# Kernel optimization log

Measured on AMD Instinct MI355X. Metric: run time of the kernel, lower is better.

## Reference

```python
import jax, jax.numpy as jnp
import numpy as np

N_EMBD = 2048
N_HEAD = 16
N_HIDDEN = 5632  # find_multiple(int(2*4*2048/3), 256)
EPS = 1e-5
BETA = 1.0


def rmsnorm(x, scale):
    # mean of squares computed in fp32 as in the torch code
    norm = jnp.mean(x.astype(jnp.float32) ** 2, axis=-1, keepdims=True)
    x_normed = x * jax.lax.rsqrt(norm + EPS)
    return (scale * x_normed).astype(x.dtype)


def setup_inputs() -> dict:
    key = jax.random.key(0)
    ks = jax.random.split(key, 9)
    B, T, C = 1, 2048, N_EMBD
    s = lambda k, shape, fan: jax.random.normal(k, shape, jnp.float32) * (1.0 / np.sqrt(fan))
    return {
        "x": jax.random.normal(ks[0], (B, T, C), jnp.float32),
        "alibi": jax.random.normal(ks[1], (N_HEAD, T, T), jnp.float32),
        "w_attn": s(ks[2], (C, 3 * C), C),   # c_attn weight (in, out) layout
        "w_proj": s(ks[3], (C, C), C),
        "w_fc1": s(ks[4], (C, N_HIDDEN), C),
        "w_fc2": s(ks[5], (C, N_HIDDEN), C),
        "w_mlp_proj": s(ks[6], (N_HIDDEN, C), N_HIDDEN),
        "rms1_scale": jnp.ones((C,), jnp.float32),
        "rms2_scale": jnp.ones((C,), jnp.float32),
    }


def attention(x, alibi, w_attn, w_proj):
    B, T, C = x.shape
    hd = C // N_HEAD
    qkv = x @ w_attn  # [B,T,3C]
    q, k, v = jnp.split(qkv, 3, axis=-1)
    q = q.reshape(B, T, N_HEAD, hd).transpose(0, 2, 1, 3)  # [B,H,T,hd]
    k = k.reshape(B, T, N_HEAD, hd).transpose(0, 2, 1, 3)
    v = v.reshape(B, T, N_HEAD, hd).transpose(0, 2, 1, 3)
    scale = 1.0 / np.sqrt(hd)
    scores = jnp.einsum("bhqd,bhkd->bhqk", q, k) * scale + BETA * alibi  # [B,H,T,T]
    causal = jnp.tril(jnp.ones((T, T), bool))
    scores = jnp.where(causal, scores, -jnp.inf)
    attn = jax.nn.softmax(scores, axis=-1)
    y = jnp.einsum("bhqk,bhkd->bhqd", attn, v)
    y = y.transpose(0, 2, 1, 3).reshape(B, T, C)
    return y @ w_proj


def mlp(x, w_fc1, w_fc2, w_mlp_proj):
    return (jax.nn.silu(x @ w_fc1) * (x @ w_fc2)) @ w_mlp_proj


def reference(x, alibi, w_attn, w_proj, w_fc1, w_fc2, w_mlp_proj, rms1_scale, rms2_scale):
    x = x + attention(rmsnorm(x, rms1_scale), alibi, w_attn, w_proj)
    x = x + mlp(rmsnorm(x, rms2_scale), w_fc1, w_fc2, w_mlp_proj)
    return x
```

## Files before the change

### kernel.cpp

```cpp
#include <hip/hip_runtime.h>
#include <stdint.h>

typedef __attribute__((ext_vector_type(4))) float f32x4;
typedef __attribute__((ext_vector_type(8))) __bf16 bf8_t;
typedef __attribute__((ext_vector_type(8))) uint16_t u16x8;

typedef __attribute__((address_space(1))) uint8_t as1_u8;
typedef __attribute__((address_space(3))) uint8_t as3_u8;

__device__ inline void async_copy16(const void* g, void* l) {
  __builtin_amdgcn_global_load_lds((const as1_u8*)g, (as3_u8*)l, 16, 0, 0);
}

__device__ inline uint16_t f2bf(float f) {
  uint32_t u = __builtin_bit_cast(uint32_t, f);
  u = (u + 0x7fff + ((u >> 16) & 1)) >> 16;
  return (uint16_t)u;
}
__device__ inline float bf2f(uint16_t h) {
  uint32_t u = ((uint32_t)h) << 16;
  return __builtin_bit_cast(float, u);
}
__device__ inline int swz(int r) { return (((r & 7) ^ ((r >> 3) & 7)) << 4); }
__device__ inline int vswz(int r) { return ((r & 7) << 4); }

__global__ __launch_bounds__(256) void rmsnorm_kernel(const float* __restrict__ X,
                                                      const float* __restrict__ S,
                                                      uint16_t* __restrict__ O) {
  const int row = blockIdx.x;
  const int tid = threadIdx.x;
  const float* xr = X + (size_t)row * 2048;
  float4 v1 = ((const float4*)xr)[tid * 2];
  float4 v2 = ((const float4*)xr)[tid * 2 + 1];
  float ss = v1.x * v1.x + v1.y * v1.y + v1.z * v1.z + v1.w * v1.w +
             v2.x * v2.x + v2.y * v2.y + v2.z * v2.z + v2.w * v2.w;
  #pragma unroll
  for (int m = 1; m < 64; m <<= 1) ss += __shfl_xor(ss, m);
  __shared__ float wsum[4];
  if ((tid & 63) == 0) wsum[tid >> 6] = ss;
  __syncthreads();
  float tot = wsum[0] + wsum[1] + wsum[2] + wsum[3];
  float inv = rsqrtf(tot * (1.0f / 2048.0f) + 1e-5f);
  const int base = tid * 8;
  const float* sc = S + base;
  float xs[8] = {v1.x, v1.y, v1.z, v1.w, v2.x, v2.y, v2.z, v2.w};
  u16x8 o;
  #pragma unroll
  for (int j = 0; j < 8; j++) o[j] = f2bf(xs[j] * inv * sc[j]);
  *(u16x8*)(O + (size_t)row * 2048 + base) = o;
}

__device__ inline void transpose_tile2(const float* __restrict__ W, uint16_t* __restrict__ WT,
                                       int K, int N, int bx, int by, int tid, int catoff) {
  __shared__ float tile[64][65];
  const int n0 = bx * 64, k0 = by * 64;
  const int lr = tid >> 4;
  const int lc = (tid & 15) * 4;
  #pragma unroll
  for (int i = 0; i < 4; i++) {
    const float4 v = *(const float4*)&W[(size_t)(k0 + lr + i * 16) * N + n0 + lc];
    tile[lr + i * 16][lc] = v.x;
    tile[lr + i * 16][lc + 1] = v.y;
    tile[lr + i * 16][lc + 2] = v.z;
    tile[lr + i * 16][lc + 3] = v.w;
  }
  __syncthreads();
  const int tn = tid >> 3;
  const int tk = (tid & 7) * 8;
  #pragma unroll
  for (int i = 0; i < 2; i++) {
    u16x8 o;
    #pragma unroll
    for (int j = 0; j < 8; j++) o[j] = f2bf(tile[tk + j][tn + i * 32]);
    const int n = n0 + tn + i * 32;
    const int row = (catoff < 0) ? n : (((n >> 4) << 5) + catoff + (n & 15));
    *(u16x8*)&WT[(size_t)row * K + k0 + tk] = o;
  }
}

__global__ __launch_bounds__(256) void transpose_all(
    const float* __restrict__ w_attn, const float* __restrict__ w_proj,
    const float* __restrict__ w_fc1, const float* __restrict__ w_fc2,
    const float* __restrict__ w_mp,
    uint16_t* __restrict__ wt_attn, uint16_t* __restrict__ wt_proj,
    uint16_t* __restrict__ wt_cat, uint16_t* __restrict__ wt_mp) {
  int idx = blockIdx.x;
  const int tid = threadIdx.x;
  if (idx < 3072) {
    transpose_tile2(w_attn, wt_attn, 2048, 6144, idx % 96, idx / 96, tid, -1);
  } else if (idx < 4096) {
    idx -= 3072;
    transpose_tile2(w_proj, wt_proj, 2048, 2048, idx % 32, idx / 32, tid, -1);
  } else if (idx < 6912) {
    idx -= 4096;
    transpose_tile2(w_fc1, wt_cat, 2048, 5632, idx % 88, idx / 88, tid, 0);
  } else if (idx < 9728) {
    idx -= 6912;
    transpose_tile2(w_fc2, wt_cat, 2048, 5632, idx % 88, idx / 88, tid, 16);
  } else {
    idx -= 9728;
    transpose_tile2(w_mp, wt_mp, 5632, 2048, idx % 32, idx / 32, tid, -1);
  }
}

__global__ __launch_bounds__(256) void transpose_v(const uint16_t* __restrict__ qkv,
                                                   uint16_t* __restrict__ vT) {
  __shared__ uint16_t tile[64][68];
  const int t0 = blockIdx.x * 64;
  const int c0 = blockIdx.y * 64;
  const int tid = threadIdx.x;
  const int lr = tid >> 3;
  const int lc = (tid & 7) * 8;
  #pragma unroll
  for (int i = 0; i < 2; i++) {
    const int r = lr + i * 32;
    u16x8 v = *(const u16x8*)&qkv[(size_t)(t0 + r) * 6144 + 4096 + c0 + lc];
    #pragma unroll
    for (int j = 0; j < 8; j++) tile[lc + j][r] = v[j];
  }
  __syncthreads();
  #pragma unroll
  for (int i = 0; i < 2; i++) {
    const int c = lr + i * 32;
    u16x8 o = *(const u16x8*)&tile[c][lc];
    *(u16x8*)&vT[(size_t)(c0 + c) * 2048 + t0 + lc] = o;
  }
}

enum { EPI_BF16 = 0, EPI_ADDF32 = 1, EPI_SILUMUL = 2 };

__device__ inline void gemm_epi(int EPI, void* Cout, const void* RES, size_t idx, float v) {
  if (EPI == EPI_BF16) {
    ((uint16_t*)Cout)[idx] = f2bf(v);
  } else if (EPI == EPI_ADDF32) {
    ((float*)Cout)[idx] = ((const float*)RES)[idx] + v;
  } else {
    const float g = bf2f(((const uint16_t*)RES)[idx]);
    const float sg = g / (1.0f + __expf(-g));
    ((uint16_t*)Cout)[idx] = f2bf(sg * v);
  }
}

template <int EPI>
__global__ __launch_bounds__(256, 2) void gemm_bt(const uint16_t* __restrict__ A,
                                                  const uint16_t* __restrict__ BT,
                                                  void* __restrict__ Cout,
                                                  const void* __restrict__ RES,
                                                  int M, int N, int K) {
  __shared__ uint16_t As[128 * 64];
  __shared__ uint16_t Bs[128 * 64];
  const int tid = threadIdx.x;
  const int lane = tid & 63;
  const int w = tid >> 6;
  const int l15 = lane & 15, l4 = lane >> 4;
  const int m0 = blockIdx.y * 128, n0 = blockIdx.x * 128;
  const int wr = w >> 1, wc = w & 1;

  f32x4 acc[4][4];
  #pragma unroll
  for (int i = 0; i < 4; i++)
    #pragma unroll
    for (int j = 0; j < 4; j++) acc[i][j] = 0.0f;

  for (int kk = 0; kk < K; kk += 64) {
    __syncthreads();
    #pragma unroll
    for (int s = 0; s < 4; s++) {
      const int bu = s * 256 + w * 64;
      const int u = bu + lane;
      const int row = u >> 3;
      const int ch = (u & 7) ^ (row & 7);
      async_copy16(A + (size_t)(m0 + row) * K + kk + ch * 8, (char*)As + bu * 16);
      async_copy16(BT + (size_t)(n0 + row) * K + kk + ch * 8, (char*)Bs + bu * 16);
    }
    __syncthreads();
    bf8_t a[4][2], b[4][2];
    #pragma unroll
    for (int mi = 0; mi < 4; mi++)
      #pragma unroll
      for (int ks = 0; ks < 2; ks++) {
        const int R = wr * 64 + mi * 16 + l15;
        a[mi][ks] = *(const bf8_t*)((const char*)As + R * 128 + (((ks * 4 + l4) ^ (R & 7)) * 16));
      }
    #pragma unroll
    for (int ni = 0; ni < 4; ni++)
      #pragma unroll
      for (int ks = 0; ks < 2; ks++) {
        const int R = wc * 64 + ni * 16 + l15;
        b[ni][ks] = *(const bf8_t*)((const char*)Bs + R * 128 + (((ks * 4 + l4) ^ (R & 7)) * 16));
      }
    #pragma unroll
    for (int mi = 0; mi < 4; mi++)
      #pragma unroll
      for (int ni = 0; ni < 4; ni++)
        #pragma unroll
        for (int ks = 0; ks < 2; ks++)
          acc[mi][ni] = __builtin_amdgcn_mfma_f32_16x16x32_bf16(a[mi][ks], b[ni][ks],
                                                                acc[mi][ni], 0, 0, 0);
  }

  #pragma unroll
  for (int mi = 0; mi < 4; mi++) {
    #pragma unroll
    for (int ni = 0; ni < 4; ni++) {
      #pragma unroll
      for (int r = 0; r < 4; r++) {
        const int row = m0 + wr * 64 + mi * 16 + l4 * 4 + r;
        const int col = n0 + wc * 64 + ni * 16 + l15;
        gemm_epi(EPI, Cout, RES, (size_t)row * N + col, acc[mi][ni][r]);
      }
    }
  }
}

__global__ __launch_bounds__(256, 2) void gemm_cat(const uint16_t* __restrict__ A,
                                                   const uint16_t* __restrict__ BT,
                                                   uint16_t* __restrict__ Cout,
                                                   int M, int K) {
  __shared__ uint16_t As[128 * 64];
  __shared__ uint16_t Bs[128 * 64];
  const int tid = threadIdx.x;
  const int lane = tid & 63;
  const int w = tid >> 6;
  const int l15 = lane & 15, l4 = lane >> 4;
  const int m0 = blockIdx.y * 128, n0 = blockIdx.x * 128;
  const int wr = w >> 1, wc = w & 1;

  f32x4 acc[4][4];
  #pragma unroll
  for (int i = 0; i < 4; i++)
    #pragma unroll
    for (int j = 0; j < 4; j++) acc[i][j] = 0.0f;

  for (int kk = 0; kk < K; kk += 64) {
    __syncthreads();
    #pragma unroll
    for (int s = 0; s < 4; s++) {
      const int bu = s * 256 + w * 64;
      const int u = bu + lane;
      const int row = u >> 3;
      const int ch = (u & 7) ^ (row & 7);
      async_copy16(A + (size_t)(m0 + row) * K + kk + ch * 8, (char*)As + bu * 16);
      async_copy16(BT + (size_t)(n0 + row) * K + kk + ch * 8, (char*)Bs + bu * 16);
    }
    __syncthreads();
    bf8_t a[4][2], b[4][2];
    #pragma unroll
    for (int mi = 0; mi < 4; mi++)
      #pragma unroll
      for (int ks = 0; ks < 2; ks++) {
        const int R = wr * 64 + mi * 16 + l15;
        a[mi][ks] = *(const bf8_t*)((const char*)As + R * 128 + (((ks * 4 + l4) ^ (R & 7)) * 16));
      }
    #pragma unroll
    for (int ni = 0; ni < 4; ni++)
      #pragma unroll
      for (int ks = 0; ks < 2; ks++) {
        const int R = wc * 64 + ni * 16 + l15;
        b[ni][ks] = *(const bf8_t*)((const char*)Bs + R * 128 + (((ks * 4 + l4) ^ (R & 7)) * 16));
      }
    #pragma unroll
    for (int mi = 0; mi < 4; mi++)
      #pragma unroll
      for (int ni = 0; ni < 4; ni++)
        #pragma unroll
        for (int ks = 0; ks < 2; ks++)
          acc[mi][ni] = __builtin_amdgcn_mfma_f32_16x16x32_bf16(a[mi][ks], b[ni][ks],
                                                                acc[mi][ni], 0, 0, 0);
  }

  #pragma unroll
  for (int mi = 0; mi < 4; mi++) {
    #pragma unroll
    for (int p = 0; p < 2; p++) {
      const int col = n0 / 2 + ((wc * 4 + 2 * p) >> 1) * 16 + l15;
      #pragma unroll
      for (int r = 0; r < 4; r++) {
        const int row = m0 + wr * 64 + mi * 16 + l4 * 4 + r;
        const float g = acc[mi][2 * p][r];
        const float h = acc[mi][2 * p + 1][r];
        const float sg = g / (1.0f + __expf(-g));
        Cout[(size_t)row * 5632 + col] = f2bf(sg * h);
      }
    }
  }
}

template <int EPI>
__global__ __launch_bounds__(256, 3) void gemm_bt64(const uint16_t* __restrict__ A,
                                                    const uint16_t* __restrict__ BT,
                                                    void* __restrict__ Cout,
                                                    const void* __restrict__ RES,
                                                    int M, int N, int K) {
  __shared__ uint16_t As[128 * 64];
  __shared__ uint16_t Bs[64 * 64];
  const int tid = threadIdx.x;
  const int lane = tid & 63;
  const int w = tid >> 6;
  const int l15 = lane & 15, l4 = lane >> 4;
  const int m0 = blockIdx.y * 128, n0 = blockIdx.x * 64;

  f32x4 acc[2][4];
  #pragma unroll
  for (int i = 0; i < 2; i++)
    #pragma unroll
    for (int j = 0; j < 4; j++) acc[i][j] = 0.0f;

  for (int kk = 0; kk < K; kk += 64) {
    __syncthreads();
    #pragma unroll
    for (int s = 0; s < 4; s++) {
      const int bu = s * 256 + w * 64;
      const int u = bu + lane;
      const int row = u >> 3;
      const int ch = (u & 7) ^ (row & 7);
      async_copy16(A + (size_t)(m0 + row) * K + kk + ch * 8, (char*)As + bu * 16);
    }
    #pragma unroll
    for (int s = 0; s < 2; s++) {
      const int bu = s * 256 + w * 64;
      const int u = bu + lane;
      const int row = u >> 3;
      const int ch = (u & 7) ^ (row & 7);
      async_copy16(BT + (size_t)(n0 + row) * K + kk + ch * 8, (char*)Bs + bu * 16);
    }
    __syncthreads();
    bf8_t a[2][2], b[4][2];
    #pragma unroll
    for (int mi = 0; mi < 2; mi++)
      #pragma unroll
      for (int ks = 0; ks < 2; ks++) {
        const int R = w * 32 + mi * 16 + l15;
        a[mi][ks] = *(const bf8_t*)((const char*)As + R * 128 + (((ks * 4 + l4) ^ (R & 7)) * 16));
      }
    #pragma unroll
    for (int ni = 0; ni < 4; ni++)
      #pragma unroll
      for (int ks = 0; ks < 2; ks++) {
        const int R = ni * 16 + l15;
        b[ni][ks] = *(const bf8_t*)((const char*)Bs + R * 128 + (((ks * 4 + l4) ^ (R & 7)) * 16));
      }
    #pragma unroll
    for (int mi = 0; mi < 2; mi++)
      #pragma unroll
      for (int ni = 0; ni < 4; ni++)
        #pragma unroll
        for (int ks = 0; ks < 2; ks++)
          acc[mi][ni] = __builtin_amdgcn_mfma_f32_16x16x32_bf16(a[mi][ks], b[ni][ks],
                                                                acc[mi][ni], 0, 0, 0);
  }

  #pragma unroll
  for (int mi = 0; mi < 2; mi++) {
    #pragma unroll
    for (int ni = 0; ni < 4; ni++) {
      #pragma unroll
      for (int r = 0; r < 4; r++) {
        const int row = m0 + w * 32 + mi * 16 + l4 * 4 + r;
        const int col = n0 + ni * 16 + l15;
        gemm_epi(EPI, Cout, RES, (size_t)row * N + col, acc[mi][ni][r]);
      }
    }
  }
}

#define PART_STRIDE (64 * 128 + 128)
__global__ __launch_bounds__(256, 2) void attn_part(const uint16_t* __restrict__ qkv,
                                                    const uint16_t* __restrict__ vT,
                                                    const float* __restrict__ alibi,
                                                    float* __restrict__ part) {
  const int p = blockIdx.x;
  const int qt = 31 - blockIdx.y;
  const int h = blockIdx.z;
  const int c = (qt + 4) >> 2;
  const int start = p * c;
  const int end = min((p + 1) * c, qt + 1);
  if (start >= end) return;

  const int tid = threadIdx.x;
  const int lane = tid & 63;
  const int w = tid >> 6;
  const int l15 = lane & 15, l4 = lane >> 4;

  __shared__ uint16_t Ks[2][64 * 128];
  __shared__ uint16_t Vs[2][128 * 64];
  __shared__ uint16_t Ps[4][16 * 64];

  const float scale = 0.08838834764831845f;

  auto stage = [&](int kv0, int b) {
    #pragma unroll
    for (int i = 0; i < 4; i++) {
      const int u = tid + i * 256;
      const int r = u >> 4;
      const int cc = (u & 15) ^ ((r & 7) ^ ((r >> 3) & 7));
      async_copy16(qkv + (size_t)(kv0 + r) * 6144 + 2048 + h * 128 + cc * 8,
                   (char*)Ks[b] + u * 16);
    }
    #pragma unroll
    for (int i = 0; i < 4; i++) {
      const int u = tid + i * 256;
      const int r = u >> 3;
      const int cc = (u & 7) ^ (r & 7);
      async_copy16(vT + (size_t)(h * 128 + r) * 2048 + kv0 + cc * 8,
                   (char*)Vs[b] + u * 16);
    }
  };
  auto load_al = [&](int kv0, float (&al)[4][4]) {
    #pragma unroll
    for (int r = 0; r < 4; r++) {
      const size_t rowb = ((size_t)h * 2048 + (qt * 64 + w * 16 + l4 * 4 + r)) * 2048;
      #pragma unroll
      for (int nf = 0; nf < 4; nf++)
        al[nf][r] = alibi[rowb + kv0 + nf * 16 + l15];
    }
  };

  const int qrow = qt * 64 + w * 16 + l15;
  bf8_t qf[4];
  #pragma unroll
  for (int kc = 0; kc < 4; kc++)
    qf[kc] = *(const bf8_t*)(qkv + (size_t)qrow * 6144 + h * 128 + kc * 32 + l4 * 8);

  f32x4 accy[8];
  #pragma unroll
  for (int i = 0; i < 8; i++) accy[i] = 0.0f;
  float mrun[4], lrun[4];
  #pragma unroll
  for (int r = 0; r < 4; r++) { mrun[r] = -1e30f; lrun[r] = 0.0f; }

  stage(start * 64, 0);
  float al[4][4];
  load_al(start * 64, al);

  for (int kvt = start; kvt < end; kvt++) {
    const int b = (kvt - start) & 1;
    const int kv0 = kvt * 64;
    __syncthreads();

    const int kvn = (kvt + 1 < end) ? (kvt + 1) : kvt;
    float aln[4][4];
    load_al(kvn * 64, aln);
    stage(kvn * 64, b ^ 1);

    float s[4][4];
    #pragma unroll
    for (int nf = 0; nf < 4; nf++) {
      f32x4 sa = 0.0f;
      const int krow = nf * 16 + l15;
      __builtin_amdgcn_s_setprio(1);
      #pragma unroll
      for (int kc = 0; kc < 4; kc++) {
        bf8_t kb = *(const bf8_t*)((const char*)Ks[b] +
                                   ((krow * 256 + kc * 64 + l4 * 16) ^ swz(krow)));
        sa = __builtin_amdgcn_mfma_f32_16x16x32_bf16(qf[kc], kb, sa, 0, 0, 0);
      }
      __builtin_amdgcn_s_setprio(0);
      const int kvcol = kv0 + nf * 16 + l15;
      #pragma unroll
      for (int r = 0; r < 4; r++) {
        const int q = qt * 64 + w * 16 + l4 * 4 + r;
        float sv = sa[r] * scale + al[nf][r];
        if (kvcol > q) sv = -1e30f;
        s[nf][r] = sv;
      }
    }

    #pragma unroll
    for (int r = 0; r < 4; r++) {
      float rm = fmaxf(fmaxf(s[0][r], s[1][r]), fmaxf(s[2][r], s[3][r]));
      rm = fmaxf(rm, __shfl_xor(rm, 1));
      rm = fmaxf(rm, __shfl_xor(rm, 2));
      rm = fmaxf(rm, __shfl_xor(rm, 4));
      rm = fmaxf(rm, __shfl_xor(rm, 8));
      const float mnew = fmaxf(mrun[r], rm);
      const float alpha = __expf(mrun[r] - mnew);
      mrun[r] = mnew;
      float rs = 0.0f;
      #pragma unroll
      for (int nf = 0; nf < 4; nf++) {
        const float pp = __expf(s[nf][r] - mnew);
        s[nf][r] = pp;
        rs += pp;
      }
      rs += __shfl_xor(rs, 1);
      rs += __shfl_xor(rs, 2);
      rs += __shfl_xor(rs, 4);
      rs += __shfl_xor(rs, 8);
      lrun[r] = lrun[r] * alpha + rs;
      #pragma unroll
      for (int df = 0; df < 8; df++) accy[df][r] *= alpha;
    }

    #pragma unroll
    for (int nf = 0; nf < 4; nf++) {
      #pragma unroll
      for (int r = 0; r < 4; r++) {
        const int rq = l4 * 4 + r;
        const int bo = (rq * 128 + (nf * 16 + l15) * 2) ^ vswz(rq);
        *(uint16_t*)((char*)Ps[w] + bo) = f2bf(s[nf][r]);
      }
    }

    __builtin_amdgcn_s_setprio(1);
    #pragma unroll
    for (int kk = 0; kk < 2; kk++) {
      bf8_t pa = *(const bf8_t*)((const char*)Ps[w] +
                                 ((l15 * 128 + kk * 64 + l4 * 16) ^ vswz(l15)));
      #pragma unroll
      for (int df = 0; df < 8; df++) {
        const int vr = df * 16 + l15;
        bf8_t vb = *(const bf8_t*)((const char*)Vs[b] +
                                   ((vr * 128 + kk * 64 + l4 * 16) ^ vswz(vr)));
        accy[df] = __builtin_amdgcn_mfma_f32_16x16x32_bf16(pa, vb, accy[df], 0, 0, 0);
      }
    }
    __builtin_amdgcn_s_setprio(0);

    #pragma unroll
    for (int nf = 0; nf < 4; nf++)
      #pragma unroll
      for (int r = 0; r < 4; r++) al[nf][r] = aln[nf][r];
  }

  float* pb = part + (size_t)(((h * 32 + qt) * 4) + p) * PART_STRIDE;
  #pragma unroll
  for (int df = 0; df < 8; df++) {
    #pragma unroll
    for (int r = 0; r < 4; r++) {
      const int row = w * 16 + l4 * 4 + r;
      pb[row * 128 + df * 16 + l15] = accy[df][r];
    }
  }
  if (l15 == 0) {
    #pragma unroll
    for (int r = 0; r < 4; r++) {
      const int row = w * 16 + l4 * 4 + r;
      pb[8192 + row] = mrun[r];
      pb[8192 + 64 + row] = lrun[r];
    }
  }
}

__global__ __launch_bounds__(256) void attn_merge(const float* __restrict__ part,
                                                  uint16_t* __restrict__ Y) {
  const int qt = blockIdx.x;
  const int h = blockIdx.y;
  const int c = (qt + 4) >> 2;
  const int cnt = (qt + c) / c;
  const int tid = threadIdx.x;
  const int row = tid >> 2;
  const int cg = (tid & 3) * 32;

  const float* pb = part + (size_t)((h * 32 + qt) * 4) * PART_STRIDE;

  float m_p[4], w_p[4];
  float M = -1e30f;
  for (int p = 0; p < cnt; p++) {
    m_p[p] = pb[p * PART_STRIDE + 8192 + row];
    M = fmaxf(M, m_p[p]);
  }
  float L = 0.0f;
  for (int p = 0; p < cnt; p++) {
    w_p[p] = __expf(m_p[p] - M);
    L += w_p[p] * pb[p * PART_STRIDE + 8192 + 64 + row];
  }
  const float invL = 1.0f / L;

  uint16_t* yr = Y + (size_t)(qt * 64 + row) * 2048 + h * 128 + cg;
  #pragma unroll
  for (int j = 0; j < 32; j += 8) {
    f32x4 s0 = 0.0f, s1 = 0.0f;
    for (int p = 0; p < cnt; p++) {
      const float* ap = pb + p * PART_STRIDE + row * 128 + cg + j;
      s0 += w_p[p] * *(const f32x4*)ap;
      s1 += w_p[p] * *(const f32x4*)(ap + 4);
    }
    u16x8 o;
    #pragma unroll
    for (int e = 0; e < 4; e++) { o[e] = f2bf(s0[e] * invL); o[e + 4] = f2bf(s1[e] * invL); }
    *(u16x8*)(yr + j) = o;
  }
}

extern "C" void kernel_launch(void* const* d_in, const int* in_sizes, int n_in,
                              void* d_out, int out_size, void* d_ws, size_t ws_size,
                              hipStream_t stream) {
  const float* x      = (const float*)d_in[0];
  const float* alibi  = (const float*)d_in[1];
  const float* w_attn = (const float*)d_in[2];
  const float* w_proj = (const float*)d_in[3];
  const float* w_fc1  = (const float*)d_in[4];
  const float* w_fc2  = (const float*)d_in[5];
  const float* w_mp   = (const float*)d_in[6];
  const float* rms1   = (const float*)d_in[7];
  const float* rms2   = (const float*)d_in[8];
  float* out = (float*)d_out;

  char* ws = (char*)d_ws;
  uint16_t* xn      = (uint16_t*)(ws + 0);
  uint16_t* qkv     = (uint16_t*)(ws + 8388608);
  uint16_t* y       = (uint16_t*)(ws + 33554432);
  uint16_t* hbuf    = (uint16_t*)(ws + 65011712);
  uint16_t* wt_attn = (uint16_t*)(ws + 88080384);
  uint16_t* wt_proj = (uint16_t*)(ws + 113246208);
  uint16_t* wt_cat  = (uint16_t*)(ws + 121634816);
  uint16_t* wt_mp   = (uint16_t*)(ws + 167772160);
  uint16_t* vT      = (uint16_t*)(ws + 190840832);
  float*    part    = (float*)(ws + 199229440);

  transpose_all<<<12544, 256, 0, stream>>>(w_attn, w_proj, w_fc1, w_fc2, w_mp,
                                           wt_attn, wt_proj, wt_cat, wt_mp);

  rmsnorm_kernel<<<2048, 256, 0, stream>>>(x, rms1, xn);

  gemm_bt<EPI_BF16><<<dim3(6144 / 128, 2048 / 128), 256, 0, stream>>>(
      xn, wt_attn, qkv, nullptr, 2048, 6144, 2048);

  transpose_v<<<dim3(32, 32), 256, 0, stream>>>(qkv, vT);

  attn_part<<<dim3(4, 32, 16), 256, 0, stream>>>(qkv, vT, alibi, part);

  attn_merge<<<dim3(32, 16), 256, 0, stream>>>(part, y);

  gemm_bt64<EPI_ADDF32><<<dim3(2048 / 64, 2048 / 128), 256, 0, stream>>>(
      y, wt_proj, out, x, 2048, 2048, 2048);

  rmsnorm_kernel<<<2048, 256, 0, stream>>>(out, rms2, xn);

  gemm_cat<<<dim3(11264 / 128, 2048 / 128), 256, 0, stream>>>(
      xn, wt_cat, hbuf, 2048, 2048);

  gemm_bt64<EPI_ADDF32><<<dim3(2048 / 64, 2048 / 128), 256, 0, stream>>>(
      hbuf, wt_mp, out, out, 2048, 2048, 5632);
}
```

Baseline: 477.5 us.

## Raise GEMM occupancy, split MFMA loads by k-step, store attention partials in bf16

The GEMM kernels now load A/B fragments one k-substep at a time instead of both at once, which cuts live registers, and their launch bound is raised to 3 blocks per CU. The split-K attention partial outputs are stored as bf16 instead of fp32, halving the partial-buffer traffic between attn_part and attn_merge. The bf16 partials add rounding error before the merge, and the higher occupancy target could force register spills.

```diff
diff --git a/kernel.cpp b/kernel.cpp
--- a/kernel.cpp
+++ b/kernel.cpp
@@ -23,6 +23,8 @@
 }
 __device__ inline int swz(int r) { return (((r & 7) ^ ((r >> 3) & 7)) << 4); }
 __device__ inline int vswz(int r) { return ((r & 7) << 4); }
+
+#define PART_BYTES (64 * 128 * 2 + 128 * 4)
 
 __global__ __launch_bounds__(256) void rmsnorm_kernel(const float* __restrict__ X,
                                                       const float* __restrict__ S,
@@ -142,7 +144,7 @@
 }
 
 template <int EPI>
-__global__ __launch_bounds__(256, 2) void gemm_bt(const uint16_t* __restrict__ A,
+__global__ __launch_bounds__(256, 3) void gemm_bt(const uint16_t* __restrict__ A,
                                                   const uint16_t* __restrict__ BT,
                                                   void* __restrict__ Cout,
                                                   const void* __restrict__ RES,
@@ -174,29 +176,25 @@
       async_copy16(BT + (size_t)(n0 + row) * K + kk + ch * 8, (char*)Bs + bu * 16);
     }
     __syncthreads();
-    bf8_t a[4][2], b[4][2];
-    #pragma unroll
-    for (int mi = 0; mi < 4; mi++)
-      #pragma unroll
-      for (int ks = 0; ks < 2; ks++) {
+    #pragma unroll
+    for (int ks = 0; ks < 2; ks++) {
+      bf8_t a[4], b[4];
+      #pragma unroll
+      for (int mi = 0; mi < 4; mi++) {
         const int R = wr * 64 + mi * 16 + l15;
-        a[mi][ks] = *(const bf8_t*)((const char*)As + R * 128 + (((ks * 4 + l4) ^ (R & 7)) * 16));
-      }
-    #pragma unroll
-    for (int ni = 0; ni < 4; ni++)
-      #pragma unroll
-      for (int ks = 0; ks < 2; ks++) {
+        a[mi] = *(const bf8_t*)((const char*)As + R * 128 + (((ks * 4 + l4) ^ (R & 7)) * 16));
+      }
+      #pragma unroll
+      for (int ni = 0; ni < 4; ni++) {
         const int R = wc * 64 + ni * 16 + l15;
-        b[ni][ks] = *(const bf8_t*)((const char*)Bs + R * 128 + (((ks * 4 + l4) ^ (R & 7)) * 16));
-      }
-    #pragma unroll
-    for (int mi = 0; mi < 4; mi++)
-      #pragma unroll
-      for (int ni = 0; ni < 4; ni++)
+        b[ni] = *(const bf8_t*)((const char*)Bs + R * 128 + (((ks * 4 + l4) ^ (R & 7)) * 16));
+      }
+      #pragma unroll
+      for (int mi = 0; mi < 4; mi++)
         #pragma unroll
-        for (int ks = 0; ks < 2; ks++)
-          acc[mi][ni] = __builtin_amdgcn_mfma_f32_16x16x32_bf16(a[mi][ks], b[ni][ks],
-                                                                acc[mi][ni], 0, 0, 0);
+        for (int ni = 0; ni < 4; ni++)
+          acc[mi][ni] = __builtin_amdgcn_mfma_f32_16x16x32_bf16(a[mi], b[ni], acc[mi][ni], 0, 0, 0);
+    }
   }
 
   #pragma unroll
@@ -213,7 +211,7 @@
   }
 }
 
-__global__ __launch_bounds__(256, 2) void gemm_cat(const uint16_t* __restrict__ A,
+__global__ __launch_bounds__(256, 3) void gemm_cat(const uint16_t* __restrict__ A,
                                                    const uint16_t* __restrict__ BT,
                                                    uint16_t* __restrict__ Cout,
                                                    int M, int K) {
@@ -244,29 +242,25 @@
       async_copy16(BT + (size_t)(n0 + row) * K + kk + ch * 8, (char*)Bs + bu * 16);
     }
     __syncthreads();
-    bf8_t a[4][2], b[4][2];
-    #pragma unroll
-    for (int mi = 0; mi < 4; mi++)
-      #pragma unroll
-      for (int ks = 0; ks < 2; ks++) {
+    #pragma unroll
+    for (int ks = 0; ks < 2; ks++) {
+      bf8_t a[4], b[4];
+      #pragma unroll
+      for (int mi = 0; mi < 4; mi++) {
         const int R = wr * 64 + mi * 16 + l15;
-        a[mi][ks] = *(const bf8_t*)((const char*)As + R * 128 + (((ks * 4 + l4) ^ (R & 7)) * 16));
-      }
-    #pragma unroll
-    for (int ni = 0; ni < 4; ni++)
-      #pragma unroll
-      for (int ks = 0; ks < 2; ks++) {
+        a[mi] = *(const bf8_t*)((const char*)As + R * 128 + (((ks * 4 + l4) ^ (R & 7)) * 16));
+      }
+      #pragma unroll
+      for (int ni = 0; ni < 4; ni++) {
         const int R = wc * 64 + ni * 16 + l15;
-        b[ni][ks] = *(const bf8_t*)((const char*)Bs + R * 128 + (((ks * 4 + l4) ^ (R & 7)) * 16));
-      }
-    #pragma unroll
-    for (int mi = 0; mi < 4; mi++)
-      #pragma unroll
-      for (int ni = 0; ni < 4; ni++)
+        b[ni] = *(const bf8_t*)((const char*)Bs + R * 128 + (((ks * 4 + l4) ^ (R & 7)) * 16));
+      }
+      #pragma unroll
+      for (int mi = 0; mi < 4; mi++)
         #pragma unroll
-        for (int ks = 0; ks < 2; ks++)
-          acc[mi][ni] = __builtin_amdgcn_mfma_f32_16x16x32_bf16(a[mi][ks], b[ni][ks],
-                                                                acc[mi][ni], 0, 0, 0);
+        for (int ni = 0; ni < 4; ni++)
+          acc[mi][ni] = __builtin_amdgcn_mfma_f32_16x16x32_bf16(a[mi], b[ni], acc[mi][ni], 0, 0, 0);
+    }
   }
 
   #pragma unroll
@@ -364,11 +358,10 @@
   }
 }
 
-#define PART_STRIDE (64 * 128 + 128)
 __global__ __launch_bounds__(256, 2) void attn_part(const uint16_t* __restrict__ qkv,
                                                     const uint16_t* __restrict__ vT,
                                                     const float* __restrict__ alibi,
-                                                    float* __restrict__ part) {
+                                                    char* __restrict__ part) {
   const int p = blockIdx.x;
   const int qt = 31 - blockIdx.y;
   const int h = blockIdx.z;
@@ -523,26 +516,28 @@
       for (int r = 0; r < 4; r++) al[nf][r] = aln[nf][r];
   }
 
-  float* pb = part + (size_t)(((h * 32 + qt) * 4) + p) * PART_STRIDE;
+  char* pb = part + (size_t)(((h * 32 + qt) * 4) + p) * PART_BYTES;
+  uint16_t* pa = (uint16_t*)pb;
   #pragma unroll
   for (int df = 0; df < 8; df++) {
     #pragma unroll
     for (int r = 0; r < 4; r++) {
       const int row = w * 16 + l4 * 4 + r;
-      pb[row * 128 + df * 16 + l15] = accy[df][r];
-    }
-  }
+      pa[row * 128 + df * 16 + l15] = f2bf(accy[df][r]);
+    }
+  }
+  float* pml = (float*)(pb + 16384);
   if (l15 == 0) {
     #pragma unroll
     for (int r = 0; r < 4; r++) {
       const int row = w * 16 + l4 * 4 + r;
-      pb[8192 + row] = mrun[r];
-      pb[8192 + 64 + row] = lrun[r];
-    }
-  }
-}
-
-__global__ __launch_bounds__(256) void attn_merge(const float* __restrict__ part,
+      pml[row] = mrun[r];
+      pml[64 + row] = lrun[r];
+    }
+  }
+}
+
+__global__ __launch_bounds__(256) void attn_merge(const char* __restrict__ part,
                                                   uint16_t* __restrict__ Y) {
   const int qt = blockIdx.x;
   const int h = blockIdx.y;
@@ -552,33 +547,33 @@
   const int row = tid >> 2;
   const int cg = (tid & 3) * 32;
 
-  const float* pb = part + (size_t)((h * 32 + qt) * 4) * PART_STRIDE;
+  const char* pb = part + (size_t)((h * 32 + qt) * 4) * PART_BYTES;
 
   float m_p[4], w_p[4];
   float M = -1e30f;
   for (int p = 0; p < cnt; p++) {
-    m_p[p] = pb[p * PART_STRIDE + 8192 + row];
+    m_p[p] = ((const float*)(pb + p * PART_BYTES + 16384))[row];
     M = fmaxf(M, m_p[p]);
   }
   float L = 0.0f;
   for (int p = 0; p < cnt; p++) {
     w_p[p] = __expf(m_p[p] - M);
-    L += w_p[p] * pb[p * PART_STRIDE + 8192 + 64 + row];
+    L += w_p[p] * ((const float*)(pb + p * PART_BYTES + 16384))[64 + row];
   }
   const float invL = 1.0f / L;
 
   uint16_t* yr = Y + (size_t)(qt * 64 + row) * 2048 + h * 128 + cg;
   #pragma unroll
   for (int j = 0; j < 32; j += 8) {
-    f32x4 s0 = 0.0f, s1 = 0.0f;
+    float s[8] = {0, 0, 0, 0, 0, 0, 0, 0};
     for (int p = 0; p < cnt; p++) {
-      const float* ap = pb + p * PART_STRIDE + row * 128 + cg + j;
-      s0 += w_p[p] * *(const f32x4*)ap;
-      s1 += w_p[p] * *(const f32x4*)(ap + 4);
+      const u16x8 v = *(const u16x8*)(pb + p * PART_BYTES + (size_t)(row * 128 + cg + j) * 2);
+      #pragma unroll
+      for (int e = 0; e < 8; e++) s[e] += w_p[p] * bf2f(v[e]);
     }
     u16x8 o;
     #pragma unroll
-    for (int e = 0; e < 4; e++) { o[e] = f2bf(s0[e] * invL); o[e + 4] = f2bf(s1[e] * invL); }
+    for (int e = 0; e < 8; e++) o[e] = f2bf(s[e] * invL);
     *(u16x8*)(yr + j) = o;
   }
 }
@@ -607,7 +602,7 @@
   uint16_t* wt_cat  = (uint16_t*)(ws + 121634816);
   uint16_t* wt_mp   = (uint16_t*)(ws + 167772160);
   uint16_t* vT      = (uint16_t*)(ws + 190840832);
-  float*    part    = (float*)(ws + 199229440);
+  char*     part    = (char*)(ws + 199229440);
 
   transpose_all<<<12544, 256, 0, stream>>>(w_attn, w_proj, w_fc1, w_fc2, w_mp,
                                            wt_attn, wt_proj, wt_cat, wt_mp);
```

Result: faster. 452.5 us, median of 2 (-5.2%).
